# Performance work log

Measured on AMD Instinct MI355X. Metric: run time of the kernel, lower is better.

The kernel has to match this reference:

```python
import jax, jax.numpy as jnp
import numpy as np

K_HOPS = 2  # number_layers


def _gcn_norm(edge_index, edge_weight, num_nodes):
    # add self loops with weight 1 (PyG gcn_norm default, fill_value=1)
    row, col = edge_index[0], edge_index[1]
    loop = jnp.arange(num_nodes, dtype=edge_index.dtype)
    row = jnp.concatenate([row, loop])
    col = jnp.concatenate([col, loop])
    w = jnp.concatenate([edge_weight, jnp.ones((num_nodes,), edge_weight.dtype)])
    deg = jax.ops.segment_sum(w, col, num_segments=num_nodes)
    dinv = jnp.where(deg > 0, jax.lax.rsqrt(deg), 0.0)
    norm = dinv[row] * w * dinv[col]
    return row, col, norm


def setup_inputs() -> dict:
    key = jax.random.key(0)
    k1, k2, k3, k4 = jax.random.split(key, 4)
    N, E, F_IN, F_OUT = 100000, 1600000, 256, 40
    x = jax.random.normal(k1, (N, F_IN), dtype=jnp.float32)
    edge_index = jax.random.randint(k2, (2, E), 0, N, dtype=jnp.int64)
    edge_attr = jax.random.uniform(k3, (E,), dtype=jnp.float32)
    W = jax.random.normal(k4, (F_OUT, F_IN), dtype=jnp.float32) * (1.0 / np.sqrt(F_IN))
    b = jnp.zeros((F_OUT,), dtype=jnp.float32)
    return {"x": x, "edge_index": edge_index, "edge_attr": edge_attr, "W": W, "b": b}


def reference(x, edge_index, edge_attr, W, b):
    N = x.shape[0]
    row, col, norm = _gcn_norm(edge_index, edge_attr, N)
    for _ in range(K_HOPS):
        x = jax.ops.segment_sum(norm[:, None] * x[row], col, num_segments=N)
    out = x @ W.T + b           # SGConv final linear
    out = jax.nn.relu(out)      # dropout is a no-op in eval mode
    return jax.nn.log_softmax(out, axis=-1)
```

## Files before the change

kernel.cpp:

```cpp
#include <hip/hip_runtime.h>
#include <hip/hip_bf16.h>
#include <math.h>

#define TF_IN   256
#define TF_OUT  40
#define NCH2    5
#define BCAP    48
#define WQ      32767.0f
#define BIN_SHIFT 8
#define MAXBINS 512
#define EPB 4096


struct us8 { ushort4 a, b; };

__device__ inline float bf2f(unsigned short u) {
    union { unsigned int i; float f; } t; t.i = ((unsigned int)u) << 16; return t.f;
}
__device__ inline unsigned short f2bf(float f) {
    union { float f; unsigned int i; } t; t.f = f;
    unsigned int r = t.i + 0x7FFF + ((t.i >> 16) & 1);
    return (unsigned short)(r >> 16);
}

__device__ inline void acc8(float* acc, float v, const us8& h) {
    acc[0] += v * bf2f(h.a.x); acc[1] += v * bf2f(h.a.y);
    acc[2] += v * bf2f(h.a.z); acc[3] += v * bf2f(h.a.w);
    acc[4] += v * bf2f(h.b.x); acc[5] += v * bf2f(h.b.y);
    acc[6] += v * bf2f(h.b.z); acc[7] += v * bf2f(h.b.w);
}

__global__ void zero_kernel(int* __restrict__ a, int na, int* __restrict__ b, int nb) {
    int i = blockIdx.x * blockDim.x + threadIdx.x;
    if (i < na) a[i] = 0;
    if (i < nb) b[i] = 0;
}

__global__ __launch_bounds__(256) void partition_kernel(
        const int* __restrict__ row, const int* __restrict__ col,
        const float* __restrict__ w, int* __restrict__ binCnt,
        uint2* __restrict__ bins, int E, int bincap, int nbins) {
    __shared__ int hist[MAXBINS];
    __shared__ unsigned int cursor[MAXBINS];
    int tid = threadIdx.x;
    int base = (int)blockIdx.x * EPB;

    for (int i = tid; i < nbins; i += 256) hist[i] = 0;

    int   ec[16], er[16];
    float ev[16];
#pragma unroll
    for (int i = 0; i < 16; ++i) ec[i] = -1;
#pragma unroll
    for (int q = 0; q < 4; ++q) {
        int e = base + (q * 256 + tid) * 4;
        if (e + 4 <= E) {
            int4   c4 = *(const int4*)(col + e);
            int4   r4 = *(const int4*)(row + e);
            float4 w4 = *(const float4*)(w + e);
            ec[q * 4 + 0] = c4.x; ec[q * 4 + 1] = c4.y; ec[q * 4 + 2] = c4.z; ec[q * 4 + 3] = c4.w;
            er[q * 4 + 0] = r4.x; er[q * 4 + 1] = r4.y; er[q * 4 + 2] = r4.z; er[q * 4 + 3] = r4.w;
            ev[q * 4 + 0] = w4.x; ev[q * 4 + 1] = w4.y; ev[q * 4 + 2] = w4.z; ev[q * 4 + 3] = w4.w;
        } else {
            for (int j = 0; j < 4; ++j) {
                int ee = e + j;
                if (ee < E) { ec[q * 4 + j] = col[ee]; er[q * 4 + j] = row[ee]; ev[q * 4 + j] = w[ee]; }
            }
        }
    }
    __syncthreads();

#pragma unroll
    for (int i = 0; i < 16; ++i)
        if (ec[i] >= 0) atomicAdd(&hist[ec[i] >> BIN_SHIFT], 1);
    __syncthreads();

    for (int bq = tid; bq < nbins; bq += 256) {
        int hc = hist[bq];
        unsigned int g = (unsigned int)bq * (unsigned int)bincap;
        if (hc > 0) g += (unsigned int)atomicAdd(&binCnt[bq], hc);
        cursor[bq] = g;
    }
    __syncthreads();

#pragma unroll
    for (int i = 0; i < 16; ++i) {
        if (ec[i] >= 0) {
            int bq = ec[i] >> BIN_SHIFT;
            unsigned int p = atomicAdd(&cursor[bq], 1u);
            if (p < (unsigned int)(bq + 1) * (unsigned int)bincap) {
                unsigned int wq = (unsigned int)(ev[i] * WQ + 0.5f);
                uint2 ent; ent.x = ((unsigned int)er[i] << 15) | wq; ent.y = (unsigned int)ec[i];
                bins[p] = ent;
            }
        }
    }
}

__global__ __launch_bounds__(256) void fused_gemm_binscatter_kernel(
        const float* __restrict__ x, const float* __restrict__ W,
        unsigned short* __restrict__ h, int N, int nbins,
        const int* __restrict__ binCnt, const uint2* __restrict__ bins, int bincap,
        int* __restrict__ cnt, unsigned int* __restrict__ bucket) {
    __shared__ float4 xs[128][8];
    __shared__ float4 wsm[40][9];
    int tid = threadIdx.x;

    if ((int)blockIdx.x < nbins) {
        int b = blockIdx.x;
        int mb = binCnt[b]; if (mb > bincap) mb = bincap;
        const uint2* src = bins + (size_t)b * bincap;
        for (int i = tid; i < mb; i += 256) {
            uint2 e = src[i];
            int c = (int)e.y;
            int pos = atomicAdd(&cnt[c], 1);
            if (pos < BCAP) bucket[(size_t)c * BCAP + pos] = e.x;
        }
    } else {
        int q = (int)blockIdx.x - nbins;
        int ng = tid >> 2;
        int jg = tid & 3;
        int j0 = jg * 10;
        int nodeBase = q * 128;
        int sk = (ng >> 1) & 7;

        float acc[2][10];
#pragma unroll
        for (int i = 0; i < 2; ++i)
#pragma unroll
            for (int j = 0; j < 10; ++j) acc[i][j] = 0.f;

        const float4* x4 = (const float4*)x;
        const float4* W4 = (const float4*)W;

        float4 px[4], pw0, pw1;
        int xn[4], xc[4];
#pragma unroll
        for (int i = 0; i < 4; ++i) {
            int idx = tid + i * 256;
            xn[i] = idx >> 3; xc[i] = idx & 7;
        }
        int wj0 = tid >> 3, wc0 = tid & 7;
        int wj1 = (tid + 256) >> 3, wc1 = (tid + 256) & 7;

#pragma unroll
        for (int i = 0; i < 4; ++i) {
            int gn = nodeBase + xn[i];
            px[i] = (gn < N) ? x4[(size_t)gn * (TF_IN / 4) + xc[i]]
                             : make_float4(0.f, 0.f, 0.f, 0.f);
        }
        pw0 = W4[(size_t)wj0 * (TF_IN / 4) + wc0];
        if (tid < 64) pw1 = W4[(size_t)wj1 * (TF_IN / 4) + wc1];

        for (int kt = 0; kt < 8; ++kt) {
            __syncthreads();
#pragma unroll
            for (int i = 0; i < 4; ++i)
                xs[xn[i]][xc[i] ^ ((xn[i] >> 2) & 7)] = px[i];
            wsm[wj0][wc0] = pw0;
            if (tid < 64) wsm[wj1][wc1] = pw1;
            __syncthreads();

            if (kt < 7) {
                int kb4n = (kt + 1) * 8;
#pragma unroll
                for (int i = 0; i < 4; ++i) {
                    int gn = nodeBase + xn[i];
                    px[i] = (gn < N) ? x4[(size_t)gn * (TF_IN / 4) + kb4n + xc[i]]
                                     : make_float4(0.f, 0.f, 0.f, 0.f);
                }
                pw0 = W4[(size_t)wj0 * (TF_IN / 4) + kb4n + wc0];
                if (tid < 64) pw1 = W4[(size_t)wj1 * (TF_IN / 4) + kb4n + wc1];
            }

#pragma unroll 2
            for (int c4 = 0; c4 < 8; ++c4) {
                int phys = c4 ^ sk;
                float4 xv0 = xs[ng * 2][phys];
                float4 xv1 = xs[ng * 2 + 1][phys];
#pragma unroll
                for (int jj = 0; jj < 10; ++jj) {
                    float4 wv = wsm[j0 + jj][c4];
                    acc[0][jj] += xv0.x * wv.x + xv0.y * wv.y + xv0.z * wv.z + xv0.w * wv.w;
                    acc[1][jj] += xv1.x * wv.x + xv1.y * wv.y + xv1.z * wv.z + xv1.w * wv.w;
                }
            }
        }

#pragma unroll
        for (int i = 0; i < 2; ++i) {
            int gn = nodeBase + ng * 2 + i;
            if (gn < N) {
                ushort2* hp2 = (ushort2*)(h + (size_t)gn * TF_OUT + j0);
#pragma unroll
                for (int p = 0; p < 5; ++p) {
                    ushort2 o;
                    o.x = f2bf(acc[i][2 * p]);
                    o.y = f2bf(acc[i][2 * p + 1]);
                    hp2[p] = o;
                }
            }
        }
    }
}

__global__ void deg_kernel(const unsigned int* __restrict__ bucket, const int* __restrict__ cnt,
                           float* __restrict__ dinv, int N) {
    int n = blockIdx.x * blockDim.x + threadIdx.x;
    if (n >= N) return;
    int m = cnt[n]; if (m > BCAP) m = BCAP;
    const unsigned int* b = bucket + (size_t)n * BCAP;
    unsigned int si = 0;
    int k = 0;
    for (; k + 4 <= m; k += 4) {
        uint4 e4 = *(const uint4*)(b + k);
        si += (e4.x & 0x7FFF) + (e4.y & 0x7FFF) + (e4.z & 0x7FFF) + (e4.w & 0x7FFF);
    }
    for (; k < m; ++k) si += b[k] & 0x7FFF;
    float s = 1.0f + (float)si * (1.0f / WQ);
    dinv[n] = rsqrtf(s);
}

__device__ inline void stage_rv(int g, int chunk, int m,
                                const unsigned int* __restrict__ b,
                                const float* __restrict__ dinv,
                                int rs[64][BCAP + 1], float vs[64][BCAP + 1]) {
    int k0 = chunk * 10;
    unsigned int e[10];
#pragma unroll
    for (int i = 0; i < 10; ++i) {
        int k = k0 + i;
        e[i] = (k < m) ? b[k] : 0u;
    }
    float dv[10];
#pragma unroll
    for (int i = 0; i < 10; ++i) dv[i] = dinv[e[i] >> 15];
#pragma unroll
    for (int i = 0; i < 10; ++i) {
        int k = k0 + i;
        if (k < m) {
            rs[g][k] = (int)(e[i] >> 15);
            vs[g][k] = dv[i] * ((float)(e[i] & 0x7FFF) * (1.0f / WQ));
        }
    }
}

__device__ inline void gather_lds(float* acc, const us8* __restrict__ hin,
                                  int g, int chunk, int m,
                                  const int rs[64][BCAP + 1], const float vs[64][BCAP + 1]) {
    int k = 0;
    for (; k + 8 <= m; k += 8) {
        us8 h0 = hin[(size_t)rs[g][k + 0] * NCH2 + chunk];
        us8 h1 = hin[(size_t)rs[g][k + 1] * NCH2 + chunk];
        us8 h2 = hin[(size_t)rs[g][k + 2] * NCH2 + chunk];
        us8 h3 = hin[(size_t)rs[g][k + 3] * NCH2 + chunk];
        us8 h4 = hin[(size_t)rs[g][k + 4] * NCH2 + chunk];
        us8 h5 = hin[(size_t)rs[g][k + 5] * NCH2 + chunk];
        us8 h6 = hin[(size_t)rs[g][k + 6] * NCH2 + chunk];
        us8 h7 = hin[(size_t)rs[g][k + 7] * NCH2 + chunk];
        acc8(acc, vs[g][k + 0], h0); acc8(acc, vs[g][k + 1], h1);
        acc8(acc, vs[g][k + 2], h2); acc8(acc, vs[g][k + 3], h3);
        acc8(acc, vs[g][k + 4], h4); acc8(acc, vs[g][k + 5], h5);
        acc8(acc, vs[g][k + 6], h6); acc8(acc, vs[g][k + 7], h7);
    }
    if (k + 4 <= m) {
        us8 h0 = hin[(size_t)rs[g][k + 0] * NCH2 + chunk];
        us8 h1 = hin[(size_t)rs[g][k + 1] * NCH2 + chunk];
        us8 h2 = hin[(size_t)rs[g][k + 2] * NCH2 + chunk];
        us8 h3 = hin[(size_t)rs[g][k + 3] * NCH2 + chunk];
        acc8(acc, vs[g][k + 0], h0); acc8(acc, vs[g][k + 1], h1);
        acc8(acc, vs[g][k + 2], h2); acc8(acc, vs[g][k + 3], h3);
        k += 4;
    }
    for (; k < m; ++k) {
        us8 hv = hin[(size_t)rs[g][k] * NCH2 + chunk];
        acc8(acc, vs[g][k], hv);
    }
}

__global__ __launch_bounds__(320) void hop_bf_kernel(
        const us8* __restrict__ hin, us8* __restrict__ hout,
        const int* __restrict__ cnt, const unsigned int* __restrict__ bucket,
        const float* __restrict__ dinv, int N) {
    __shared__ int   rs[64][BCAP + 1];
    __shared__ float vs[64][BCAP + 1];
    int tid = threadIdx.x;
    int g = tid / NCH2;
    int chunk = tid - g * NCH2;
    int node = blockIdx.x * 64 + g;

    int m = 0;
    float d = 0.f;
    if (node < N) {
        m = cnt[node]; if (m > BCAP) m = BCAP;
        d = dinv[node];
        stage_rv(g, chunk, m, bucket + (size_t)node * BCAP, dinv, rs, vs);
    }
    __syncthreads();
    if (node >= N) return;

    us8 a = hin[(size_t)node * NCH2 + chunk];
    float acc[8];
    acc[0] = bf2f(a.a.x) * d; acc[1] = bf2f(a.a.y) * d;
    acc[2] = bf2f(a.a.z) * d; acc[3] = bf2f(a.a.w) * d;
    acc[4] = bf2f(a.b.x) * d; acc[5] = bf2f(a.b.y) * d;
    acc[6] = bf2f(a.b.z) * d; acc[7] = bf2f(a.b.w) * d;

    gather_lds(acc, hin, g, chunk, m, rs, vs);

    us8 o;
    o.a.x = f2bf(acc[0] * d); o.a.y = f2bf(acc[1] * d);
    o.a.z = f2bf(acc[2] * d); o.a.w = f2bf(acc[3] * d);
    o.b.x = f2bf(acc[4] * d); o.b.y = f2bf(acc[5] * d);
    o.b.z = f2bf(acc[6] * d); o.b.w = f2bf(acc[7] * d);
    hout[(size_t)node * NCH2 + chunk] = o;
}

__global__ __launch_bounds__(320) void hop2_epi_kernel(
        const us8* __restrict__ hin, float4* __restrict__ out,
        const int* __restrict__ cnt, const unsigned int* __restrict__ bucket,
        const float* __restrict__ dinv, const float* __restrict__ bias, int N) {
    __shared__ int   rs[64][BCAP + 1];
    __shared__ float vs[64][BCAP + 1];
    __shared__ float redm[320];
    __shared__ float reds[320];
    int tid = threadIdx.x;
    int g = tid / NCH2;
    int chunk = tid - g * NCH2;
    int node = blockIdx.x * 64 + g;
    bool valid = node < N;

    int m = 0;
    float d = 0.f;
    if (valid) {
        m = cnt[node]; if (m > BCAP) m = BCAP;
        d = dinv[node];
        stage_rv(g, chunk, m, bucket + (size_t)node * BCAP, dinv, rs, vs);
    }
    __syncthreads();

    float acc[8];
#pragma unroll
    for (int j = 0; j < 8; ++j) acc[j] = 0.f;
    if (valid) {
        us8 a = hin[(size_t)node * NCH2 + chunk];
        acc[0] = bf2f(a.a.x) * d; acc[1] = bf2f(a.a.y) * d;
        acc[2] = bf2f(a.a.z) * d; acc[3] = bf2f(a.a.w) * d;
        acc[4] = bf2f(a.b.x) * d; acc[5] = bf2f(a.b.y) * d;
        acc[6] = bf2f(a.b.z) * d; acc[7] = bf2f(a.b.w) * d;
        gather_lds(acc, hin, g, chunk, m, rs, vs);
    }

    float v[8];
    float lm = -1e30f;
    if (valid) {
#pragma unroll
        for (int j = 0; j < 8; ++j) {
            float t2 = acc[j] * d + bias[chunk * 8 + j];
            t2 = fmaxf(t2, 0.f);
            v[j] = t2;
            lm = fmaxf(lm, t2);
        }
    }
    redm[tid] = lm;
    __syncthreads();
    float gm = redm[g * NCH2];
#pragma unroll
    for (int i = 1; i < NCH2; ++i) gm = fmaxf(gm, redm[g * NCH2 + i]);

    float ps = 0.f;
    if (valid) {
#pragma unroll
        for (int j = 0; j < 8; ++j) ps += __expf(v[j] - gm);
    }
    reds[tid] = ps;
    __syncthreads();
    float s = reds[g * NCH2];
#pragma unroll
    for (int i = 1; i < NCH2; ++i) s += reds[g * NCH2 + i];
    float lse = gm + __logf(s);

    if (valid) {
        float4 o0 = make_float4(v[0] - lse, v[1] - lse, v[2] - lse, v[3] - lse);
        float4 o1 = make_float4(v[4] - lse, v[5] - lse, v[6] - lse, v[7] - lse);
        out[(size_t)node * 10 + chunk * 2]     = o0;
        out[(size_t)node * 10 + chunk * 2 + 1] = o1;
    }
}

extern "C" void kernel_launch(void* const* d_in, const int* in_sizes, int n_in,
                              void* d_out, int out_size, void* d_ws, size_t ws_size,
                              hipStream_t stream) {
    const float* x  = (const float*)d_in[0];
    const int*   ei = (const int*)d_in[1];
    const float* ew = (const float*)d_in[2];
    const float* W  = (const float*)d_in[3];
    const float* b  = (const float*)d_in[4];

    const int F_out = in_sizes[4];
    const int F_in  = in_sizes[3] / F_out;
    const int N     = in_sizes[0] / F_in;
    const int E     = in_sizes[2];
    const int* row = ei;
    const int* col = ei + E;

    char* ws = (char*)d_ws;
    size_t off = 0;
    auto alloc = [&](size_t bytes) {
        void* p = ws + off;
        off += (bytes + 255) & ~(size_t)255;
        return p;
    };

    int*          cnt    = (int*)          alloc((size_t)N * 4);
    float*        dinv   = (float*)        alloc((size_t)N * 4);
    unsigned int* bucket = (unsigned int*) alloc((size_t)N * BCAP * 4);
    unsigned short* h0   = (unsigned short*)alloc((size_t)N * TF_OUT * 2);
    unsigned short* h1   = (unsigned short*)alloc((size_t)N * TF_OUT * 2);
    int nbins = (N + (1 << BIN_SHIFT) - 1) >> BIN_SHIFT;
    int* binCnt = (int*)alloc((size_t)nbins * 4);

    size_t outBytes = (size_t)N * F_out * 4;
    int bincap = (int)(outBytes / ((size_t)nbins * 8));
    uint2* bins = (uint2*)d_out;

    const int tb = 256;
    hipLaunchKernelGGL(zero_kernel, dim3((N + tb - 1) / tb), dim3(tb), 0, stream,
                       cnt, N, binCnt, nbins);

    int partBlocks = (E + EPB - 1) / EPB;
    hipLaunchKernelGGL(partition_kernel, dim3(partBlocks), dim3(tb), 0, stream,
                       row, col, ew, binCnt, bins, E, bincap, nbins);

    int gemmBlocks = (N + 127) / 128;
    hipLaunchKernelGGL(fused_gemm_binscatter_kernel, dim3(nbins + gemmBlocks), dim3(256),
                       0, stream, x, W, h0, N, nbins, binCnt, bins, bincap, cnt, bucket);

    hipLaunchKernelGGL(deg_kernel, dim3((N + tb - 1) / tb), dim3(tb), 0, stream,
                       bucket, cnt, dinv, N);

    int hopBlocks = (N + 63) / 64;
    hipLaunchKernelGGL(hop_bf_kernel, dim3(hopBlocks), dim3(320), 0, stream,
                       (const us8*)h0, (us8*)h1, cnt, bucket, dinv, N);

    hipLaunchKernelGGL(hop2_epi_kernel, dim3(hopBlocks), dim3(320), 0, stream,
                       (const us8*)h1, (float4*)d_out, cnt, bucket, dinv, b, N);
}
```

Measured before the change: 308.9 us.

## Use 64-node bins directly as CSR, dropping per-node bucket scatter

Shrinks the bins to 64 destination nodes, matching one hop block, and makes each hop kernel stage its bin's edges into shared memory with local atomics. This removes the global per-node bucket array, its count array and the global-atomic scatter pass. Partitioning is fused with the GEMM in one launch, and degree is computed per bin with shared atomics. In exchange each hop kernel re-reads and re-sorts the bin edges, and capacity is fixed at 1280 edges per bin, which risks overflow on skewed graphs.

```diff
diff --git a/kernel.cpp b/kernel.cpp
--- a/kernel.cpp
+++ b/kernel.cpp
@@ -7,9 +7,10 @@
 #define NCH2    5
 #define BCAP    48
 #define WQ      32767.0f
-#define BIN_SHIFT 8
-#define MAXBINS 512
+#define BIN_SHIFT 6
+#define MAXBINS 1600
 #define EPB 4096
+#define BINCAP 1280
 
 
 struct us8 { ushort4 a, b; };
@@ -30,94 +31,78 @@
     acc[6] += v * bf2f(h.b.z); acc[7] += v * bf2f(h.b.w);
 }
 
-__global__ void zero_kernel(int* __restrict__ a, int na, int* __restrict__ b, int nb) {
+__global__ void zero_kernel(int* __restrict__ a, int na) {
     int i = blockIdx.x * blockDim.x + threadIdx.x;
     if (i < na) a[i] = 0;
-    if (i < nb) b[i] = 0;
-}
-
-__global__ __launch_bounds__(256) void partition_kernel(
+}
+
+struct PartSh { int hist[MAXBINS]; unsigned int cursor[MAXBINS]; };
+struct GemmSh { float4 xs[128][8]; float4 wsm[40][9]; };
+union FusedSh { PartSh p; GemmSh g; };
+
+__global__ __launch_bounds__(256) void fused_part_gemm_kernel(
+        const float* __restrict__ x, const float* __restrict__ W,
+        unsigned short* __restrict__ h, int N, int partBlocks,
         const int* __restrict__ row, const int* __restrict__ col,
-        const float* __restrict__ w, int* __restrict__ binCnt,
-        uint2* __restrict__ bins, int E, int bincap, int nbins) {
-    __shared__ int hist[MAXBINS];
-    __shared__ unsigned int cursor[MAXBINS];
+        const float* __restrict__ w, int E,
+        int* __restrict__ binCnt, uint2* __restrict__ bins, int nbins) {
+    __shared__ FusedSh sh;
     int tid = threadIdx.x;
-    int base = (int)blockIdx.x * EPB;
-
-    for (int i = tid; i < nbins; i += 256) hist[i] = 0;
-
-    int   ec[16], er[16];
-    float ev[16];
-#pragma unroll
-    for (int i = 0; i < 16; ++i) ec[i] = -1;
-#pragma unroll
-    for (int q = 0; q < 4; ++q) {
-        int e = base + (q * 256 + tid) * 4;
-        if (e + 4 <= E) {
-            int4   c4 = *(const int4*)(col + e);
-            int4   r4 = *(const int4*)(row + e);
-            float4 w4 = *(const float4*)(w + e);
-            ec[q * 4 + 0] = c4.x; ec[q * 4 + 1] = c4.y; ec[q * 4 + 2] = c4.z; ec[q * 4 + 3] = c4.w;
-            er[q * 4 + 0] = r4.x; er[q * 4 + 1] = r4.y; er[q * 4 + 2] = r4.z; er[q * 4 + 3] = r4.w;
-            ev[q * 4 + 0] = w4.x; ev[q * 4 + 1] = w4.y; ev[q * 4 + 2] = w4.z; ev[q * 4 + 3] = w4.w;
-        } else {
-            for (int j = 0; j < 4; ++j) {
-                int ee = e + j;
-                if (ee < E) { ec[q * 4 + j] = col[ee]; er[q * 4 + j] = row[ee]; ev[q * 4 + j] = w[ee]; }
+
+    if ((int)blockIdx.x < partBlocks) {
+        int base = (int)blockIdx.x * EPB;
+        for (int i = tid; i < nbins; i += 256) sh.p.hist[i] = 0;
+
+        int   ec[16], er[16];
+        float ev[16];
+#pragma unroll
+        for (int i = 0; i < 16; ++i) ec[i] = -1;
+#pragma unroll
+        for (int q = 0; q < 4; ++q) {
+            int e = base + (q * 256 + tid) * 4;
+            if (e + 4 <= E) {
+                int4   c4 = *(const int4*)(col + e);
+                int4   r4 = *(const int4*)(row + e);
+                float4 w4 = *(const float4*)(w + e);
+                ec[q * 4 + 0] = c4.x; ec[q * 4 + 1] = c4.y; ec[q * 4 + 2] = c4.z; ec[q * 4 + 3] = c4.w;
+                er[q * 4 + 0] = r4.x; er[q * 4 + 1] = r4.y; er[q * 4 + 2] = r4.z; er[q * 4 + 3] = r4.w;
+                ev[q * 4 + 0] = w4.x; ev[q * 4 + 1] = w4.y; ev[q * 4 + 2] = w4.z; ev[q * 4 + 3] = w4.w;
+            } else {
+                for (int j = 0; j < 4; ++j) {
+                    int ee = e + j;
+                    if (ee < E) { ec[q * 4 + j] = col[ee]; er[q * 4 + j] = row[ee]; ev[q * 4 + j] = w[ee]; }
+                }
             }
         }
-    }
-    __syncthreads();
-
-#pragma unroll
-    for (int i = 0; i < 16; ++i)
-        if (ec[i] >= 0) atomicAdd(&hist[ec[i] >> BIN_SHIFT], 1);
-    __syncthreads();
-
-    for (int bq = tid; bq < nbins; bq += 256) {
-        int hc = hist[bq];
-        unsigned int g = (unsigned int)bq * (unsigned int)bincap;
-        if (hc > 0) g += (unsigned int)atomicAdd(&binCnt[bq], hc);
-        cursor[bq] = g;
-    }
-    __syncthreads();
-
-#pragma unroll
-    for (int i = 0; i < 16; ++i) {
-        if (ec[i] >= 0) {
-            int bq = ec[i] >> BIN_SHIFT;
-            unsigned int p = atomicAdd(&cursor[bq], 1u);
-            if (p < (unsigned int)(bq + 1) * (unsigned int)bincap) {
-                unsigned int wq = (unsigned int)(ev[i] * WQ + 0.5f);
-                uint2 ent; ent.x = ((unsigned int)er[i] << 15) | wq; ent.y = (unsigned int)ec[i];
-                bins[p] = ent;
+        __syncthreads();
+
+#pragma unroll
+        for (int i = 0; i < 16; ++i)
+            if (ec[i] >= 0) atomicAdd(&sh.p.hist[ec[i] >> BIN_SHIFT], 1);
+        __syncthreads();
+
+        for (int bq = tid; bq < nbins; bq += 256) {
+            int hc = sh.p.hist[bq];
+            unsigned int g = (unsigned int)bq * (unsigned int)BINCAP;
+            if (hc > 0) g += (unsigned int)atomicAdd(&binCnt[bq], hc);
+            sh.p.cursor[bq] = g;
+        }
+        __syncthreads();
+
+#pragma unroll
+        for (int i = 0; i < 16; ++i) {
+            if (ec[i] >= 0) {
+                int bq = ec[i] >> BIN_SHIFT;
+                unsigned int p = atomicAdd(&sh.p.cursor[bq], 1u);
+                if (p < (unsigned int)(bq + 1) * (unsigned int)BINCAP) {
+                    unsigned int wq = (unsigned int)(ev[i] * WQ + 0.5f);
+                    uint2 ent; ent.x = ((unsigned int)er[i] << 15) | wq; ent.y = (unsigned int)ec[i];
+                    bins[p] = ent;
+                }
             }
         }
-    }
-}
-
-__global__ __launch_bounds__(256) void fused_gemm_binscatter_kernel(
-        const float* __restrict__ x, const float* __restrict__ W,
-        unsigned short* __restrict__ h, int N, int nbins,
-        const int* __restrict__ binCnt, const uint2* __restrict__ bins, int bincap,
-        int* __restrict__ cnt, unsigned int* __restrict__ bucket) {
-    __shared__ float4 xs[128][8];
-    __shared__ float4 wsm[40][9];
-    int tid = threadIdx.x;
-
-    if ((int)blockIdx.x < nbins) {
-        int b = blockIdx.x;
-        int mb = binCnt[b]; if (mb > bincap) mb = bincap;
-        const uint2* src = bins + (size_t)b * bincap;
-        for (int i = tid; i < mb; i += 256) {
-            uint2 e = src[i];
-            int c = (int)e.y;
-            int pos = atomicAdd(&cnt[c], 1);
-            if (pos < BCAP) bucket[(size_t)c * BCAP + pos] = e.x;
-        }
     } else {
-        int q = (int)blockIdx.x - nbins;
+        int q = (int)blockIdx.x - partBlocks;
         int ng = tid >> 2;
         int jg = tid & 3;
         int j0 = jg * 10;
@@ -156,9 +141,9 @@
             __syncthreads();
 #pragma unroll
             for (int i = 0; i < 4; ++i)
-                xs[xn[i]][xc[i] ^ ((xn[i] >> 2) & 7)] = px[i];
-            wsm[wj0][wc0] = pw0;
-            if (tid < 64) wsm[wj1][wc1] = pw1;
+                sh.g.xs[xn[i]][xc[i] ^ ((xn[i] >> 2) & 7)] = px[i];
+            sh.g.wsm[wj0][wc0] = pw0;
+            if (tid < 64) sh.g.wsm[wj1][wc1] = pw1;
             __syncthreads();
 
             if (kt < 7) {
@@ -176,11 +161,11 @@
 #pragma unroll 2
             for (int c4 = 0; c4 < 8; ++c4) {
                 int phys = c4 ^ sk;
-                float4 xv0 = xs[ng * 2][phys];
-                float4 xv1 = xs[ng * 2 + 1][phys];
+                float4 xv0 = sh.g.xs[ng * 2][phys];
+                float4 xv1 = sh.g.xs[ng * 2 + 1][phys];
 #pragma unroll
                 for (int jj = 0; jj < 10; ++jj) {
-                    float4 wv = wsm[j0 + jj][c4];
+                    float4 wv = sh.g.wsm[j0 + jj][c4];
                     acc[0][jj] += xv0.x * wv.x + xv0.y * wv.y + xv0.z * wv.z + xv0.w * wv.w;
                     acc[1][jj] += xv1.x * wv.x + xv1.y * wv.y + xv1.z * wv.z + xv1.w * wv.w;
                 }
@@ -204,44 +189,40 @@
     }
 }
 
-__global__ void deg_kernel(const unsigned int* __restrict__ bucket, const int* __restrict__ cnt,
-                           float* __restrict__ dinv, int N) {
-    int n = blockIdx.x * blockDim.x + threadIdx.x;
-    if (n >= N) return;
-    int m = cnt[n]; if (m > BCAP) m = BCAP;
-    const unsigned int* b = bucket + (size_t)n * BCAP;
-    unsigned int si = 0;
-    int k = 0;
-    for (; k + 4 <= m; k += 4) {
-        uint4 e4 = *(const uint4*)(b + k);
-        si += (e4.x & 0x7FFF) + (e4.y & 0x7FFF) + (e4.z & 0x7FFF) + (e4.w & 0x7FFF);
-    }
-    for (; k < m; ++k) si += b[k] & 0x7FFF;
-    float s = 1.0f + (float)si * (1.0f / WQ);
-    dinv[n] = rsqrtf(s);
-}
-
-__device__ inline void stage_rv(int g, int chunk, int m,
-                                const unsigned int* __restrict__ b,
-                                const float* __restrict__ dinv,
-                                int rs[64][BCAP + 1], float vs[64][BCAP + 1]) {
-    int k0 = chunk * 10;
-    unsigned int e[10];
-#pragma unroll
-    for (int i = 0; i < 10; ++i) {
-        int k = k0 + i;
-        e[i] = (k < m) ? b[k] : 0u;
-    }
-    float dv[10];
-#pragma unroll
-    for (int i = 0; i < 10; ++i) dv[i] = dinv[e[i] >> 15];
-#pragma unroll
-    for (int i = 0; i < 10; ++i) {
-        int k = k0 + i;
-        if (k < m) {
-            rs[g][k] = (int)(e[i] >> 15);
-            vs[g][k] = dv[i] * ((float)(e[i] & 0x7FFF) * (1.0f / WQ));
-        }
+__global__ __launch_bounds__(256) void deg_bin_kernel(
+        const uint2* __restrict__ bins, const int* __restrict__ binCnt,
+        float* __restrict__ dinv, int N) {
+    __shared__ int wsumi[64];
+    int tid = threadIdx.x;
+    int b = blockIdx.x;
+    if (tid < 64) wsumi[tid] = 0;
+    __syncthreads();
+
+    int mb = binCnt[b]; if (mb > BINCAP) mb = BINCAP;
+    const uint2* src = bins + (size_t)b * BINCAP;
+    for (int i = tid; i < mb; i += 256) {
+        uint2 e = src[i];
+        atomicAdd(&wsumi[e.y & 63], (int)(e.x & 0x7FFF));
+    }
+    __syncthreads();
+
+    if (tid < 64) {
+        int node = b * 64 + tid;
+        if (node < N)
+            dinv[node] = rsqrtf(1.0f + (float)wsumi[tid] * (1.0f / WQ));
+    }
+}
+
+__device__ inline void stage_bin(int tid, int mb, const uint2* __restrict__ src,
+                                 const float* __restrict__ dinv,
+                                 int* lcnt, int rs[64][BCAP + 1], float vs[64][BCAP + 1]) {
+    for (int i = tid; i < mb; i += 320) {
+        uint2 e = src[i];
+        int r = (int)(e.x >> 15);
+        float v = dinv[r] * ((float)(e.x & 0x7FFF) * (1.0f / WQ));
+        int g2 = (int)(e.y & 63u);
+        int pos = atomicAdd(&lcnt[g2], 1);
+        if (pos < BCAP) { rs[g2][pos] = r; vs[g2][pos] = v; }
     }
 }
 
@@ -278,26 +259,29 @@
     }
 }
 
-__global__ __launch_bounds__(320) void hop_bf_kernel(
+__global__ __launch_bounds__(320) void hop1_kernel(
         const us8* __restrict__ hin, us8* __restrict__ hout,
-        const int* __restrict__ cnt, const unsigned int* __restrict__ bucket,
+        const uint2* __restrict__ bins, const int* __restrict__ binCnt,
         const float* __restrict__ dinv, int N) {
     __shared__ int   rs[64][BCAP + 1];
     __shared__ float vs[64][BCAP + 1];
+    __shared__ int   lcnt[64];
     int tid = threadIdx.x;
+    int b = blockIdx.x;
     int g = tid / NCH2;
     int chunk = tid - g * NCH2;
-    int node = blockIdx.x * 64 + g;
-
-    int m = 0;
-    float d = 0.f;
-    if (node < N) {
-        m = cnt[node]; if (m > BCAP) m = BCAP;
-        d = dinv[node];
-        stage_rv(g, chunk, m, bucket + (size_t)node * BCAP, dinv, rs, vs);
-    }
+    int node = b * 64 + g;
+
+    if (tid < 64) lcnt[tid] = 0;
+    __syncthreads();
+
+    int mb = binCnt[b]; if (mb > BINCAP) mb = BINCAP;
+    stage_bin(tid, mb, bins + (size_t)b * BINCAP, dinv, lcnt, rs, vs);
     __syncthreads();
     if (node >= N) return;
+
+    float d = dinv[node];
+    int m = lcnt[g]; if (m > BCAP) m = BCAP;
 
     us8 a = hin[(size_t)node * NCH2 + chunk];
     float acc[8];
@@ -318,31 +302,34 @@
 
 __global__ __launch_bounds__(320) void hop2_epi_kernel(
         const us8* __restrict__ hin, float4* __restrict__ out,
-        const int* __restrict__ cnt, const unsigned int* __restrict__ bucket,
+        const uint2* __restrict__ bins, const int* __restrict__ binCnt,
         const float* __restrict__ dinv, const float* __restrict__ bias, int N) {
     __shared__ int   rs[64][BCAP + 1];
     __shared__ float vs[64][BCAP + 1];
+    __shared__ int   lcnt[64];
     __shared__ float redm[320];
     __shared__ float reds[320];
     int tid = threadIdx.x;
+    int b = blockIdx.x;
     int g = tid / NCH2;
     int chunk = tid - g * NCH2;
-    int node = blockIdx.x * 64 + g;
+    int node = b * 64 + g;
     bool valid = node < N;
 
-    int m = 0;
+    if (tid < 64) lcnt[tid] = 0;
+    __syncthreads();
+
+    int mb = binCnt[b]; if (mb > BINCAP) mb = BINCAP;
+    stage_bin(tid, mb, bins + (size_t)b * BINCAP, dinv, lcnt, rs, vs);
+    __syncthreads();
+
+    float acc[8];
+#pragma unroll
+    for (int j = 0; j < 8; ++j) acc[j] = 0.f;
     float d = 0.f;
     if (valid) {
-        m = cnt[node]; if (m > BCAP) m = BCAP;
         d = dinv[node];
-        stage_rv(g, chunk, m, bucket + (size_t)node * BCAP, dinv, rs, vs);
-    }
-    __syncthreads();
-
-    float acc[8];
-#pragma unroll
-    for (int j = 0; j < 8; ++j) acc[j] = 0.f;
-    if (valid) {
+        int m = lcnt[g]; if (m > BCAP) m = BCAP;
         us8 a = hin[(size_t)node * NCH2 + chunk];
         acc[0] = bf2f(a.a.x) * d; acc[1] = bf2f(a.a.y) * d;
         acc[2] = bf2f(a.a.z) * d; acc[3] = bf2f(a.a.w) * d;
@@ -412,37 +399,30 @@
         return p;
     };
 
-    int*          cnt    = (int*)          alloc((size_t)N * 4);
+    int nbins = (N + (1 << BIN_SHIFT) - 1) >> BIN_SHIFT;
+
     float*        dinv   = (float*)        alloc((size_t)N * 4);
-    unsigned int* bucket = (unsigned int*) alloc((size_t)N * BCAP * 4);
+    uint2*        bins   = (uint2*)        alloc((size_t)nbins * BINCAP * 8);
     unsigned short* h0   = (unsigned short*)alloc((size_t)N * TF_OUT * 2);
     unsigned short* h1   = (unsigned short*)alloc((size_t)N * TF_OUT * 2);
-    int nbins = (N + (1 << BIN_SHIFT) - 1) >> BIN_SHIFT;
-    int* binCnt = (int*)alloc((size_t)nbins * 4);
-
-    size_t outBytes = (size_t)N * F_out * 4;
-    int bincap = (int)(outBytes / ((size_t)nbins * 8));
-    uint2* bins = (uint2*)d_out;
+    int*          binCnt = (int*)          alloc((size_t)nbins * 4);
 
     const int tb = 256;
-    hipLaunchKernelGGL(zero_kernel, dim3((N + tb - 1) / tb), dim3(tb), 0, stream,
-                       cnt, N, binCnt, nbins);
+    hipLaunchKernelGGL(zero_kernel, dim3((nbins + tb - 1) / tb), dim3(tb), 0, stream,
+                       binCnt, nbins);
 
     int partBlocks = (E + EPB - 1) / EPB;
-    hipLaunchKernelGGL(partition_kernel, dim3(partBlocks), dim3(tb), 0, stream,
-                       row, col, ew, binCnt, bins, E, bincap, nbins);
-
     int gemmBlocks = (N + 127) / 128;
-    hipLaunchKernelGGL(fused_gemm_binscatter_kernel, dim3(nbins + gemmBlocks), dim3(256),
-                       0, stream, x, W, h0, N, nbins, binCnt, bins, bincap, cnt, bucket);
-
-    hipLaunchKernelGGL(deg_kernel, dim3((N + tb - 1) / tb), dim3(tb), 0, stream,
-                       bucket, cnt, dinv, N);
-
-    int hopBlocks = (N + 63) / 64;
-    hipLaunchKernelGGL(hop_bf_kernel, dim3(hopBlocks), dim3(320), 0, stream,
-                       (const us8*)h0, (us8*)h1, cnt, bucket, dinv, N);
-
-    hipLaunchKernelGGL(hop2_epi_kernel, dim3(hopBlocks), dim3(320), 0, stream,
-                       (const us8*)h1, (float4*)d_out, cnt, bucket, dinv, b, N);
-}
+    hipLaunchKernelGGL(fused_part_gemm_kernel, dim3(partBlocks + gemmBlocks), dim3(256),
+                       0, stream, x, W, h0, N, partBlocks, row, col, ew, E,
+                       binCnt, bins, nbins);
+
+    hipLaunchKernelGGL(deg_bin_kernel, dim3(nbins), dim3(256), 0, stream,
+                       bins, binCnt, dinv, N);
+
+    hipLaunchKernelGGL(hop1_kernel, dim3(nbins), dim3(320), 0, stream,
+                       (const us8*)h0, (us8*)h1, bins, binCnt, dinv, N);
+
+    hipLaunchKernelGGL(hop2_epi_kernel, dim3(nbins), dim3(320), 0, stream,
+                       (const us8*)h1, (float4*)d_out, bins, binCnt, dinv, b, N);
+}
```

Measured after the change: 292.1 us. 5.4% less time.
